# Optimization experiments

Hardware: AMD Instinct MI355X
Metric: run time of the kernel (lower is better)

Reference implementation:

```python
import jax, jax.numpy as jnp
import numpy as np

REMOVE_FACTOR = 10000.0

def setup_inputs() -> dict:
    key = jax.random.key(0)
    k1, k2, k3, k4, k5, k6 = jax.random.split(key, 6)
    B, En, De, D_en, D_de, U = 32, 512, 64, 128, 128, 128
    return {
        "en_seq": jax.random.normal(k1, (B, En, D_en), dtype=jnp.float32),
        "de_seq": jax.random.normal(k2, (B, De, D_de), dtype=jnp.float32),
        "mask": jax.random.randint(k3, (B, En), 0, 2, dtype=jnp.int32),
        "w_en": jax.random.normal(k4, (D_en, U), dtype=jnp.float32) * (1.0 / np.sqrt(D_en)),
        "w_de": jax.random.normal(k5, (D_de, U), dtype=jnp.float32) * (1.0 / np.sqrt(D_de)),
        "nu": jax.random.normal(k6, (U, 1), dtype=jnp.float32) * (1.0 / np.sqrt(U)),
    }

def reference(en_seq, de_seq, mask, w_en, w_de, nu):
    B, En, _ = en_seq.shape
    De = de_seq.shape[1]
    m_en = mask.astype(en_seq.dtype)                      # (B, En)
    en = en_seq * m_en[:, :, None]                        # masked encoder seq
    att_en = jnp.einsum('bed,du->beu', en, w_en)          # (B, En, U)
    att_de = jnp.einsum('bdf,fu->bdu', de_seq, w_de)      # (B, De, U)
    # broadcast-add replaces the original explicit repeats: (B, De, En, U)
    co = jnp.tanh(att_en[:, None, :, :] + att_de[:, :, None, :])
    mu = jnp.einsum('bdeu,u->bde', co, nu[:, 0])          # (B, De, En)
    # Faithful reproduction of the original's flatten-layout mask bias:
    # repeat_elements(mask, De, axis=1) -> flat layout (en, de), then added
    # to mu whose flat layout is (de, en).
    bias = (jnp.repeat(m_en, De, axis=1).reshape(B, De, En) - 1.0) * REMOVE_FACTOR
    alphas = jax.nn.softmax(mu + bias, axis=-1)           # (B, De, En)
    sum_en = jnp.einsum('bde,bef->bdf', alphas, en)       # (B, De, D_en)
    return jnp.concatenate([de_seq, sum_en], axis=-1)     # (B, De, D_de + D_en)
```

## Files before the change

kernel.cpp:

```cpp
#include <hip/hip_runtime.h>


#define TWO_LOG2E 2.8853900817779268f
#define LOG2E     1.4426950408889634f

__device__ __forceinline__ float fexp2(float x){
#if __has_builtin(__builtin_amdgcn_exp2f)
  return __builtin_amdgcn_exp2f(x);
#else
  float r; asm("v_exp_f32 %0, %1" : "=v"(r) : "v"(x)); return r;
#endif
}
__device__ __forceinline__ float frcp(float x){
#if __has_builtin(__builtin_amdgcn_rcpf)
  return __builtin_amdgcn_rcpf(x);
#else
  float r; asm("v_rcp_f32 %0, %1" : "=v"(r) : "v"(x)); return r;
#endif
}

__global__ __launch_bounds__(256) void k_gemms(
    const float* __restrict__ en_seq, const float* __restrict__ de_seq,
    const float* __restrict__ w_en, const float* __restrict__ w_de,
    const int* __restrict__ mask,
    float* __restrict__ att_en, float* __restrict__ att_de_sc)
{
  __shared__ __align__(16) float Ws[64*128];
  __shared__ __align__(16) float As[32*128];
  const int bi = blockIdx.x, tid = threadIdx.x;
  const float* A; const float* W; float* O; int row0; bool masked;
  if (bi < 512) { int b = bi & 31, j = bi >> 5;
                  A = en_seq; W = w_en; O = att_en;    row0 = b*512 + j*32; masked = true; }
  else          { int q = bi - 512; int b = q & 31, jj = q >> 5;
                  A = de_seq; W = w_de; O = att_de_sc; row0 = b*64 + jj*32; masked = false; }

  const float4* A4 = (const float4*)(A + row0*128);
  float4* As4 = (float4*)As;
#pragma unroll
  for (int i = 0; i < 4; ++i) As4[tid + 256*i] = A4[tid + 256*i];

  const int c0 = (tid & 31) * 4;
  const int r0 = (tid >> 5) * 4;
  float acc[4][4] = {};

  for (int ph = 0; ph < 2; ++ph) {
    if (ph) __syncthreads();
    const float4* W4 = (const float4*)(W + ph*64*128);
    float4* Ws4 = (float4*)Ws;
#pragma unroll
    for (int i = 0; i < 8; ++i) Ws4[tid + 256*i] = W4[tid + 256*i];
    __syncthreads();
    for (int k = 0; k < 64; k += 4) {
      const int kg = ph*64 + k;
      float4 av[4], wv[4];
#pragma unroll
      for (int r = 0; r < 4; ++r) av[r] = *(const float4*)&As[(r0+r)*128 + kg];
#pragma unroll
      for (int kk = 0; kk < 4; ++kk) wv[kk] = *(const float4*)&Ws[(k+kk)*128 + c0];
#pragma unroll
      for (int r = 0; r < 4; ++r) {
        const float* ar = (const float*)&av[r];
#pragma unroll
        for (int kk = 0; kk < 4; ++kk) {
          acc[r][0] = fmaf(ar[kk], wv[kk].x, acc[r][0]);
          acc[r][1] = fmaf(ar[kk], wv[kk].y, acc[r][1]);
          acc[r][2] = fmaf(ar[kk], wv[kk].z, acc[r][2]);
          acc[r][3] = fmaf(ar[kk], wv[kk].w, acc[r][3]);
        }
      }
    }
  }
#pragma unroll
  for (int r = 0; r < 4; ++r) {
    const int row = row0 + r0 + r;
    const float m = masked ? (float)mask[row] : TWO_LOG2E;
    float4 o = { acc[r][0]*m, acc[r][1]*m, acc[r][2]*m, acc[r][3]*m };
    *(float4*)&O[row*128 + c0] = o;
  }
}

__global__ __launch_bounds__(512) void k_att(
    const float* __restrict__ att_en, const float* __restrict__ att_de_sc,
    const float* __restrict__ nu, const int* __restrict__ mask,
    const float* __restrict__ en_seq, const float* __restrict__ de_seq,
    float* __restrict__ out)
{
  __shared__ __align__(16) float smem[13864];
  float* const tile = smem;
  float* const alph = smem + 8192;
  float* const m_s  = smem + 12296;
  float* const adC  = smem + 12808;
  float* const part = smem;

  const int tid = threadIdx.x;
  const int l = tid & 63, w = tid >> 6;
  const int b = blockIdx.x & 31, dg = blockIdx.x >> 5;

  if (tid < 256) {
    const int row = tid >> 5, q = tid & 31;
    *(float4*)&adC[row*132 + q*4] =
        *(const float4*)&att_de_sc[(b*64 + dg*8 + row)*128 + q*4];
  }
  m_s[tid] = (float)mask[b*512 + tid];

  float snu = nu[l] + nu[l + 64];
#pragma unroll
  for (int off = 32; off > 0; off >>= 1) snu += __shfl_xor(snu, off, 64);
  const float S_nu = snu;

  float4 rg[4];
  const float4* AE4 = (const float4*)(att_en + (size_t)b * (512*128));
#define SLOAD(t) { _Pragma("unroll") for (int i_=0;i_<4;++i_) rg[i_] = AE4[(t)*2048 + tid + 512*i_]; }
#define SWRITE() { _Pragma("unroll") for (int i_=0;i_<4;++i_){ const int f4i_ = tid + 512*i_; \
                   const int row_ = f4i_>>5, q_ = f4i_&31; \
                   *(float4*)&tile[row_*128 + ((q_ ^ (row_&7))<<2)] = rg[i_]; } }
  SLOAD(0);
  SWRITE();
  __syncthreads();

  const int dP = l & 7, er = l >> 3;
  const int r  = w*8 + er;
  const float* adrow = adC + dP*132;
  for (int t = 0; t < 8; ++t) {
    if (t < 7) SLOAD(t+1);
    float a0=0.f, a1=0.f, a2=0.f, a3=0.f;
#pragma unroll 4
    for (int uc = 0; uc < 32; ++uc) {
      float4 ae = *(const float4*)&tile[r*128 + ((uc ^ (r&7))<<2)];
      float4 ad = *(const float4*)&adrow[uc<<2];
      float4 nv = *(const float4*)&nu[uc<<2];
      float e0 = fexp2(fmaf(ae.x, TWO_LOG2E, ad.x));
      float e1 = fexp2(fmaf(ae.y, TWO_LOG2E, ad.y));
      float e2 = fexp2(fmaf(ae.z, TWO_LOG2E, ad.z));
      float e3 = fexp2(fmaf(ae.w, TWO_LOG2E, ad.w));
      a0 = fmaf(frcp(e0 + 1.f), nv.x, a0);
      a1 = fmaf(frcp(e1 + 1.f), nv.y, a1);
      a2 = fmaf(frcp(e2 + 1.f), nv.z, a2);
      a3 = fmaf(frcp(e3 + 1.f), nv.w, a3);
    }
    alph[dP*513 + t*64 + w*8 + er] = (a0+a1)+(a2+a3);
    __syncthreads();
    if (t < 7) { SWRITE(); __syncthreads(); }
  }

  float v[8]; float mx = -3.0e38f;
#pragma unroll
  for (int t = 0; t < 8; ++t) {
    v[t] = S_nu - 2.f*alph[w*513 + t*64 + l] + (m_s[dg*64 + w*8 + t] - 1.f) * 10000.f;
    mx = fmaxf(mx, v[t]);
  }
#pragma unroll
  for (int off = 32; off > 0; off >>= 1) mx = fmaxf(mx, __shfl_xor(mx, off, 64));
  float s = 0.f, p[8];
#pragma unroll
  for (int t = 0; t < 8; ++t) { p[t] = fexp2((v[t]-mx)*LOG2E); s += p[t]; }
#pragma unroll
  for (int off = 32; off > 0; off >>= 1) s += __shfl_xor(s, off, 64);
  const float inv = frcp(s);
#pragma unroll
  for (int t = 0; t < 8; ++t)
    alph[w*513 + t*64 + l] = p[t]*inv*m_s[t*64 + l];
  __syncthreads();

  const int f0 = (l & 15) * 8, es = l >> 4;
  float acc2[8][8] = {};
  const float* enB = en_seq + (size_t)b * (512*128);
  for (int it = 0; it < 16; ++it) {
    const int e = w*64 + it*4 + es;
    float4 ev0 = *(const float4*)&enB[e*128 + f0];
    float4 ev1 = *(const float4*)&enB[e*128 + f0 + 4];
#pragma unroll
    for (int dd = 0; dd < 8; ++dd) {
      const float a = alph[dd*513 + e];
      acc2[dd][0] = fmaf(a, ev0.x, acc2[dd][0]);
      acc2[dd][1] = fmaf(a, ev0.y, acc2[dd][1]);
      acc2[dd][2] = fmaf(a, ev0.z, acc2[dd][2]);
      acc2[dd][3] = fmaf(a, ev0.w, acc2[dd][3]);
      acc2[dd][4] = fmaf(a, ev1.x, acc2[dd][4]);
      acc2[dd][5] = fmaf(a, ev1.y, acc2[dd][5]);
      acc2[dd][6] = fmaf(a, ev1.z, acc2[dd][6]);
      acc2[dd][7] = fmaf(a, ev1.w, acc2[dd][7]);
    }
  }
#pragma unroll
  for (int dd = 0; dd < 8; ++dd)
#pragma unroll
    for (int j = 0; j < 8; ++j) {
      acc2[dd][j] += __shfl_xor(acc2[dd][j], 16, 64);
      acc2[dd][j] += __shfl_xor(acc2[dd][j], 32, 64);
    }
  if (l < 16) {
#pragma unroll
    for (int dd = 0; dd < 8; ++dd) {
      float4 t0 = { acc2[dd][0], acc2[dd][1], acc2[dd][2], acc2[dd][3] };
      float4 t1 = { acc2[dd][4], acc2[dd][5], acc2[dd][6], acc2[dd][7] };
      *(float4*)&part[(w*8 + dd)*128 + f0]     = t0;
      *(float4*)&part[(w*8 + dd)*128 + f0 + 4] = t1;
    }
  }
  __syncthreads();

  if (tid < 256) {
    const int dd = tid >> 5, fq = (tid & 31) * 4;
    float4 s2 = {0.f, 0.f, 0.f, 0.f};
#pragma unroll
    for (int ww = 0; ww < 8; ++ww) {
      float4 pv = *(const float4*)&part[(ww*8 + dd)*128 + fq];
      s2.x += pv.x; s2.y += pv.y; s2.z += pv.z; s2.w += pv.w;
    }
    const int drow = b*64 + dg*8 + dd;
    *(float4*)&out[drow*256 + fq]       = *(const float4*)&de_seq[drow*128 + fq];
    *(float4*)&out[drow*256 + 128 + fq] = s2;
  }
}

extern "C" void kernel_launch(void* const* d_in, const int* in_sizes, int n_in,
                              void* d_out, int out_size, void* d_ws, size_t ws_size,
                              hipStream_t stream) {
  const float* en_seq = (const float*)d_in[0];
  const float* de_seq = (const float*)d_in[1];
  const int*   mask   = (const int*)  d_in[2];
  const float* w_en   = (const float*)d_in[3];
  const float* w_de   = (const float*)d_in[4];
  const float* nu     = (const float*)d_in[5];
  float* out = (float*)d_out;

  float* att_en    = (float*)d_ws;
  float* att_de_sc = att_en + 32*512*128;

  k_gemms<<<576, 256, 0, stream>>>(en_seq, de_seq, w_en, w_de, mask, att_en, att_de_sc);
  k_att<<<256, 512, 0, stream>>>(att_en, att_de_sc, nu, mask, en_seq, de_seq, out);
}
```

Measured before the change: 132.4 us.

## Double block sizes: split attention U-dimension across two wave halves

k_att now launches 1024 threads per block: the second half of the waves handles the upper 64 units of the tanh/nu reduction, writing into a separate alpha buffer that the softmax sums. This doubles the threads available for the transcendental-heavy score loop, but softmax and the weighted sum use only half the waves. k_gemms moves to 512-thread blocks covering 64 rows each, halving the block count and reloading the weights less often. The larger blocks raise register and LDS pressure per CU and may reduce how many blocks fit concurrently.

```diff
diff --git a/kernel.cpp b/kernel.cpp
--- a/kernel.cpp
+++ b/kernel.cpp
@@ -19,25 +19,25 @@
 #endif
 }
 
-__global__ __launch_bounds__(256) void k_gemms(
+__global__ __launch_bounds__(512) void k_gemms(
     const float* __restrict__ en_seq, const float* __restrict__ de_seq,
     const float* __restrict__ w_en, const float* __restrict__ w_de,
     const int* __restrict__ mask,
     float* __restrict__ att_en, float* __restrict__ att_de_sc)
 {
   __shared__ __align__(16) float Ws[64*128];
-  __shared__ __align__(16) float As[32*128];
+  __shared__ __align__(16) float As[64*128];
   const int bi = blockIdx.x, tid = threadIdx.x;
   const float* A; const float* W; float* O; int row0; bool masked;
-  if (bi < 512) { int b = bi & 31, j = bi >> 5;
-                  A = en_seq; W = w_en; O = att_en;    row0 = b*512 + j*32; masked = true; }
-  else          { int q = bi - 512; int b = q & 31, jj = q >> 5;
-                  A = de_seq; W = w_de; O = att_de_sc; row0 = b*64 + jj*32; masked = false; }
+  if (bi < 256) { int b = bi & 31, j = bi >> 5;
+                  A = en_seq; W = w_en; O = att_en;    row0 = b*512 + j*64; masked = true; }
+  else          { int b = bi - 256;
+                  A = de_seq; W = w_de; O = att_de_sc; row0 = b*64;         masked = false; }
 
   const float4* A4 = (const float4*)(A + row0*128);
   float4* As4 = (float4*)As;
 #pragma unroll
-  for (int i = 0; i < 4; ++i) As4[tid + 256*i] = A4[tid + 256*i];
+  for (int i = 0; i < 4; ++i) As4[tid + 512*i] = A4[tid + 512*i];
 
   const int c0 = (tid & 31) * 4;
   const int r0 = (tid >> 5) * 4;
@@ -48,7 +48,7 @@
     const float4* W4 = (const float4*)(W + ph*64*128);
     float4* Ws4 = (float4*)Ws;
 #pragma unroll
-    for (int i = 0; i < 8; ++i) Ws4[tid + 256*i] = W4[tid + 256*i];
+    for (int i = 0; i < 4; ++i) Ws4[tid + 512*i] = W4[tid + 512*i];
     __syncthreads();
     for (int k = 0; k < 64; k += 4) {
       const int kg = ph*64 + k;
@@ -79,21 +79,23 @@
   }
 }
 
-__global__ __launch_bounds__(512) void k_att(
+__global__ __launch_bounds__(1024) void k_att(
     const float* __restrict__ att_en, const float* __restrict__ att_de_sc,
     const float* __restrict__ nu, const int* __restrict__ mask,
     const float* __restrict__ en_seq, const float* __restrict__ de_seq,
     float* __restrict__ out)
 {
-  __shared__ __align__(16) float smem[13864];
-  float* const tile = smem;
-  float* const alph = smem + 8192;
-  float* const m_s  = smem + 12296;
-  float* const adC  = smem + 12808;
-  float* const part = smem;
+  __shared__ __align__(16) float smem[18080];
+  float* const tile  = smem;
+  float* const alphA = smem + 8192;
+  float* const alphB = smem + 12352;
+  float* const m_s   = smem + 16512;
+  float* const adC   = smem + 17024;
+  float* const part  = smem;
 
   const int tid = threadIdx.x;
   const int l = tid & 63, w = tid >> 6;
+  const int wl = w & 7, uh = w >> 3;
   const int b = blockIdx.x & 31, dg = blockIdx.x >> 5;
 
   if (tid < 256) {
@@ -101,17 +103,17 @@
     *(float4*)&adC[row*132 + q*4] =
         *(const float4*)&att_de_sc[(b*64 + dg*8 + row)*128 + q*4];
   }
-  m_s[tid] = (float)mask[b*512 + tid];
+  if (tid >= 512) m_s[tid - 512] = (float)mask[b*512 + tid - 512];
 
   float snu = nu[l] + nu[l + 64];
 #pragma unroll
   for (int off = 32; off > 0; off >>= 1) snu += __shfl_xor(snu, off, 64);
   const float S_nu = snu;
 
-  float4 rg[4];
+  float4 rg[2];
   const float4* AE4 = (const float4*)(att_en + (size_t)b * (512*128));
-#define SLOAD(t) { _Pragma("unroll") for (int i_=0;i_<4;++i_) rg[i_] = AE4[(t)*2048 + tid + 512*i_]; }
-#define SWRITE() { _Pragma("unroll") for (int i_=0;i_<4;++i_){ const int f4i_ = tid + 512*i_; \
+#define SLOAD(t) { _Pragma("unroll") for (int i_=0;i_<2;++i_) rg[i_] = AE4[(t)*2048 + tid + 1024*i_]; }
+#define SWRITE() { _Pragma("unroll") for (int i_=0;i_<2;++i_){ const int f4i_ = tid + 1024*i_; \
                    const int row_ = f4i_>>5, q_ = f4i_&31; \
                    *(float4*)&tile[row_*128 + ((q_ ^ (row_&7))<<2)] = rg[i_]; } }
   SLOAD(0);
@@ -119,16 +121,19 @@
   __syncthreads();
 
   const int dP = l & 7, er = l >> 3;
-  const int r  = w*8 + er;
-  const float* adrow = adC + dP*132;
+  const int r  = wl*8 + er;
+  const float* adrow = adC + dP*132 + uh*64;
+  const float* nuh   = nu + uh*64;
+  float* const alphX = uh ? alphB : alphA;
   for (int t = 0; t < 8; ++t) {
     if (t < 7) SLOAD(t+1);
     float a0=0.f, a1=0.f, a2=0.f, a3=0.f;
-#pragma unroll 4
-    for (int uc = 0; uc < 32; ++uc) {
-      float4 ae = *(const float4*)&tile[r*128 + ((uc ^ (r&7))<<2)];
+#pragma unroll
+    for (int uc = 0; uc < 16; ++uc) {
+      const int q = (uh*16 + uc) ^ er;
+      float4 ae = *(const float4*)&tile[r*128 + (q<<2)];
       float4 ad = *(const float4*)&adrow[uc<<2];
-      float4 nv = *(const float4*)&nu[uc<<2];
+      float4 nv = *(const float4*)&nuh[uc<<2];
       float e0 = fexp2(fmaf(ae.x, TWO_LOG2E, ad.x));
       float e1 = fexp2(fmaf(ae.y, TWO_LOG2E, ad.y));
       float e2 = fexp2(fmaf(ae.z, TWO_LOG2E, ad.z));
@@ -138,64 +143,69 @@
       a2 = fmaf(frcp(e2 + 1.f), nv.z, a2);
       a3 = fmaf(frcp(e3 + 1.f), nv.w, a3);
     }
-    alph[dP*513 + t*64 + w*8 + er] = (a0+a1)+(a2+a3);
+    alphX[dP*520 + t*64 + wl*8 + er] = (a0+a1)+(a2+a3);
     __syncthreads();
     if (t < 7) { SWRITE(); __syncthreads(); }
   }
 
-  float v[8]; float mx = -3.0e38f;
-#pragma unroll
-  for (int t = 0; t < 8; ++t) {
-    v[t] = S_nu - 2.f*alph[w*513 + t*64 + l] + (m_s[dg*64 + w*8 + t] - 1.f) * 10000.f;
-    mx = fmaxf(mx, v[t]);
-  }
-#pragma unroll
-  for (int off = 32; off > 0; off >>= 1) mx = fmaxf(mx, __shfl_xor(mx, off, 64));
-  float s = 0.f, p[8];
-#pragma unroll
-  for (int t = 0; t < 8; ++t) { p[t] = fexp2((v[t]-mx)*LOG2E); s += p[t]; }
-#pragma unroll
-  for (int off = 32; off > 0; off >>= 1) s += __shfl_xor(s, off, 64);
-  const float inv = frcp(s);
-#pragma unroll
-  for (int t = 0; t < 8; ++t)
-    alph[w*513 + t*64 + l] = p[t]*inv*m_s[t*64 + l];
+  if (w < 8) {
+    float v[8]; float mx = -3.0e38f;
+#pragma unroll
+    for (int t = 0; t < 8; ++t) {
+      v[t] = S_nu - 2.f*(alphA[w*520 + t*64 + l] + alphB[w*520 + t*64 + l])
+           + (m_s[dg*64 + w*8 + t] - 1.f) * 10000.f;
+      mx = fmaxf(mx, v[t]);
+    }
+#pragma unroll
+    for (int off = 32; off > 0; off >>= 1) mx = fmaxf(mx, __shfl_xor(mx, off, 64));
+    float s = 0.f, p[8];
+#pragma unroll
+    for (int t = 0; t < 8; ++t) { p[t] = fexp2((v[t]-mx)*LOG2E); s += p[t]; }
+#pragma unroll
+    for (int off = 32; off > 0; off >>= 1) s += __shfl_xor(s, off, 64);
+    const float inv = frcp(s);
+#pragma unroll
+    for (int t = 0; t < 8; ++t)
+      alphA[w*520 + t*64 + l] = p[t]*inv*m_s[t*64 + l];
+  }
   __syncthreads();
 
-  const int f0 = (l & 15) * 8, es = l >> 4;
-  float acc2[8][8] = {};
-  const float* enB = en_seq + (size_t)b * (512*128);
-  for (int it = 0; it < 16; ++it) {
-    const int e = w*64 + it*4 + es;
-    float4 ev0 = *(const float4*)&enB[e*128 + f0];
-    float4 ev1 = *(const float4*)&enB[e*128 + f0 + 4];
-#pragma unroll
-    for (int dd = 0; dd < 8; ++dd) {
-      const float a = alph[dd*513 + e];
-      acc2[dd][0] = fmaf(a, ev0.x, acc2[dd][0]);
-      acc2[dd][1] = fmaf(a, ev0.y, acc2[dd][1]);
-      acc2[dd][2] = fmaf(a, ev0.z, acc2[dd][2]);
-      acc2[dd][3] = fmaf(a, ev0.w, acc2[dd][3]);
-      acc2[dd][4] = fmaf(a, ev1.x, acc2[dd][4]);
-      acc2[dd][5] = fmaf(a, ev1.y, acc2[dd][5]);
-      acc2[dd][6] = fmaf(a, ev1.z, acc2[dd][6]);
-      acc2[dd][7] = fmaf(a, ev1.w, acc2[dd][7]);
-    }
-  }
-#pragma unroll
-  for (int dd = 0; dd < 8; ++dd)
-#pragma unroll
-    for (int j = 0; j < 8; ++j) {
-      acc2[dd][j] += __shfl_xor(acc2[dd][j], 16, 64);
-      acc2[dd][j] += __shfl_xor(acc2[dd][j], 32, 64);
-    }
-  if (l < 16) {
-#pragma unroll
-    for (int dd = 0; dd < 8; ++dd) {
-      float4 t0 = { acc2[dd][0], acc2[dd][1], acc2[dd][2], acc2[dd][3] };
-      float4 t1 = { acc2[dd][4], acc2[dd][5], acc2[dd][6], acc2[dd][7] };
-      *(float4*)&part[(w*8 + dd)*128 + f0]     = t0;
-      *(float4*)&part[(w*8 + dd)*128 + f0 + 4] = t1;
+  if (w < 8) {
+    const int f0 = (l & 15) * 8, es = l >> 4;
+    float acc2[8][8] = {};
+    const float* enB = en_seq + (size_t)b * (512*128);
+    for (int it = 0; it < 16; ++it) {
+      const int e = w*64 + it*4 + es;
+      float4 ev0 = *(const float4*)&enB[e*128 + f0];
+      float4 ev1 = *(const float4*)&enB[e*128 + f0 + 4];
+#pragma unroll
+      for (int dd = 0; dd < 8; ++dd) {
+        const float a = alphA[dd*520 + e];
+        acc2[dd][0] = fmaf(a, ev0.x, acc2[dd][0]);
+        acc2[dd][1] = fmaf(a, ev0.y, acc2[dd][1]);
+        acc2[dd][2] = fmaf(a, ev0.z, acc2[dd][2]);
+        acc2[dd][3] = fmaf(a, ev0.w, acc2[dd][3]);
+        acc2[dd][4] = fmaf(a, ev1.x, acc2[dd][4]);
+        acc2[dd][5] = fmaf(a, ev1.y, acc2[dd][5]);
+        acc2[dd][6] = fmaf(a, ev1.z, acc2[dd][6]);
+        acc2[dd][7] = fmaf(a, ev1.w, acc2[dd][7]);
+      }
+    }
+#pragma unroll
+    for (int dd = 0; dd < 8; ++dd)
+#pragma unroll
+      for (int j = 0; j < 8; ++j) {
+        acc2[dd][j] += __shfl_xor(acc2[dd][j], 16, 64);
+        acc2[dd][j] += __shfl_xor(acc2[dd][j], 32, 64);
+      }
+    if (l < 16) {
+#pragma unroll
+      for (int dd = 0; dd < 8; ++dd) {
+        float4 t0 = { acc2[dd][0], acc2[dd][1], acc2[dd][2], acc2[dd][3] };
+        float4 t1 = { acc2[dd][4], acc2[dd][5], acc2[dd][6], acc2[dd][7] };
+        *(float4*)&part[(w*8 + dd)*128 + f0]     = t0;
+        *(float4*)&part[(w*8 + dd)*128 + f0 + 4] = t1;
+      }
     }
   }
   __syncthreads();
@@ -228,6 +238,6 @@
   float* att_en    = (float*)d_ws;
   float* att_de_sc = att_en + 32*512*128;
 
-  k_gemms<<<576, 256, 0, stream>>>(en_seq, de_seq, w_en, w_de, mask, att_en, att_de_sc);
-  k_att<<<256, 512, 0, stream>>>(att_en, att_de_sc, nu, mask, en_seq, de_seq, out);
-}
+  k_gemms<<<288, 512, 0, stream>>>(en_seq, de_seq, w_en, w_de, mask, att_en, att_de_sc);
+  k_att<<<256, 1024, 0, stream>>>(att_en, att_de_sc, nu, mask, en_seq, de_seq, out);
+}
```

Result: slower. 146.6 us (+10.8%).
